# Optimization experiments

Measured on AMD Instinct MI355X. Metric: run time of the kernel, lower is better.

Reference implementation:

```python
import jax, jax.numpy as jnp
import numpy as np

B, N, D_IN, D_OUT, E = 4, 50000, 128, 128, 800000


def setup_inputs() -> dict:
    key = jax.random.key(0)
    k_x, k_w, k_b, k_r, k_c, k_v = jax.random.split(key, 6)
    stdv = 1.0 / np.sqrt(D_OUT)
    x = jax.random.normal(k_x, (B, N, D_IN), dtype=jnp.float32)
    weight = jax.random.uniform(k_w, (D_IN, D_OUT), jnp.float32, -stdv, stdv)
    bias = jax.random.uniform(k_b, (D_OUT,), jnp.float32, -stdv, stdv)
    adj_rows = jax.random.randint(k_r, (E,), 0, N, dtype=jnp.int32)
    adj_cols = jax.random.randint(k_c, (E,), 0, N, dtype=jnp.int32)
    # positive edge weights (e.g. normalized adjacency values)
    adj_vals = jax.random.uniform(k_v, (E,), jnp.float32) * (1.0 / 16.0)
    edge_index = jnp.stack([adj_rows, adj_cols]).astype(jnp.int64)  # unused (pyg_builtin=False)
    return {"input": x, "weight": weight, "bias": bias,
            "adj_vals": adj_vals, "adj_rows": adj_rows, "adj_cols": adj_cols,
            "edge_index": edge_index}


def reference(input, weight, bias, adj_vals, adj_rows, adj_cols, edge_index):
    # support = input @ W : [B, N, D_OUT]
    support = jnp.einsum('bnd,df->bnf', input, weight)

    # node_repr = sparse adj (COO) @ support, batched == torch.sparse.mm path
    def agg(s):  # s: [N, D_OUT]
        msgs = adj_vals[:, None] * s[adj_cols]          # [E, D_OUT] gather
        return jax.ops.segment_sum(msgs, adj_rows, num_segments=N)  # scatter-add

    node_repr = jax.vmap(agg)(support) + bias           # [B, N, D_OUT]
    # net_norm='none' -> no norm; activation=relu; residual=False; dropout=0
    return jax.nn.relu(node_repr)
```

## Files before the change

### kernel.cpp

```cpp
#include <hip/hip_runtime.h>
#include <hip/hip_bf16.h>

#define BB 4
#define NN 50000
#define DIN 128
#define DOUT 128
#define EE 800000
#define TOTROWS (BB * NN)
#define LDA 136

typedef unsigned short u16;
typedef unsigned int u32;

using shortx8 = __attribute__((ext_vector_type(8))) short;
using ushortx4 = __attribute__((ext_vector_type(4))) unsigned short;
using ushortx8 = __attribute__((ext_vector_type(8))) unsigned short;
using floatx4 = __attribute__((ext_vector_type(4))) float;

__device__ __forceinline__ float b2f(u16 u) {
    u32 x = ((u32)u) << 16;
    float f;
    __builtin_memcpy(&f, &x, 4);
    return f;
}

__device__ __forceinline__ u16 f2b(float f) {
    u32 x;
    __builtin_memcpy(&x, &f, 4);
    u32 r = x + 0x7fffu + ((x >> 16) & 1u);
    return (u16)(r >> 16);
}

__global__ __launch_bounds__(256)
void k_detect(const u16* __restrict__ X, const u16* __restrict__ W,
              const u16* __restrict__ Bs, const u16* __restrict__ V,
              int nx, int nw, int nb, int nv, int* __restrict__ flags) {
    __shared__ int cnt[4];
    const int t = threadIdx.x;
    const int w = t >> 6;
    const int l = t & 63;
    if (t < 4) cnt[t] = 0;
    __syncthreads();
    const u16* p = (w == 0) ? X : (w == 1) ? W : (w == 2) ? Bs : V;
    const int n  = (w == 0) ? nx : (w == 1) ? nw : (w == 2) ? nb : nv;
    int bad = 0;
    for (int k = 0; k < 4; ++k) {
        unsigned idx = 2u * (unsigned)(((unsigned long long)(l * 4 + k) *
                                        (unsigned)(n >> 1)) >> 8);
        u16 s = p[idx];
        unsigned e = (s >> 7) & 0xFF;
        bool ok = ((s & 0x7FFF) == 0) || (e >= 90 && e <= 141);
        bad += ok ? 0 : 1;
    }
    atomicAdd(&cnt[w], bad);
    __syncthreads();
    if (l == 0) flags[w] = (cnt[w] >= 77) ? 1 : 0;
}

__global__ __launch_bounds__(256)
void k_prep(const void* __restrict__ Wv, const int* __restrict__ flags,
            u16* __restrict__ Wt) {
    int t = blockIdx.x * 256 + threadIdx.x;
    if (t < DIN * DOUT) {
        int f = t >> 7, k = t & 127;
        size_t src = (size_t)k * DOUT + f;
        Wt[t] = flags[1] ? f2b(((const float*)Wv)[src]) : ((const u16*)Wv)[src];
    }
}

__global__ __launch_bounds__(256, 3)
void k_gemm(const void* __restrict__ Xv, const u16* __restrict__ Wt,
            const int* __restrict__ flags, u16* __restrict__ sup) {
    __shared__ u16 lA[128 * LDA];

    const int xf32 = flags[0];
    const int tid = threadIdx.x;
    const int wid = tid >> 6;
    const int l   = tid & 63;
    const long rowBase = (long)blockIdx.x * 128;

    if (xf32) {
        const float* Xf = (const float*)Xv;
#pragma unroll
        for (int i = 0; i < 16; ++i) {
            int elem = i * 1024 + tid * 4;
            int row = elem >> 7, col = elem & 127;
            long gRow = rowBase + row;
            ushortx4 w4 = (ushortx4){0, 0, 0, 0};
            if (gRow < TOTROWS) {
                float4 v = *(const float4*)(Xf + gRow * DIN + col);
                w4[0] = f2b(v.x); w4[1] = f2b(v.y);
                w4[2] = f2b(v.z); w4[3] = f2b(v.w);
            }
            *(ushortx4*)&lA[row * LDA + col] = w4;
        }
    } else {
        const u16* X16 = (const u16*)Xv;
#pragma unroll
        for (int i = 0; i < 8; ++i) {
            int elem = i * 2048 + tid * 8;
            int row = elem >> 7, col = elem & 127;
            long gRow = rowBase + row;
            ushortx8 w8 = (ushortx8){0, 0, 0, 0, 0, 0, 0, 0};
            if (gRow < TOTROWS)
                w8 = *(const ushortx8*)(X16 + gRow * DIN + col);
            *(ushortx8*)&lA[row * LDA + col] = w8;
        }
    }

    const int wx = wid & 1;
    const int wy = wid >> 1;
    const int q8 = (l >> 4) * 8;
    const int lm = l & 15;

    shortx8 bf[16];
#pragma unroll
    for (int nt = 0; nt < 4; ++nt) {
        const size_t Frow = (size_t)(wx * 64 + nt * 16 + lm) * DIN;
#pragma unroll
        for (int c = 0; c < 4; ++c)
            bf[nt * 4 + c] = *(const shortx8*)(Wt + Frow + 32 * c + q8);
    }

    floatx4 acc[4][4];
#pragma unroll
    for (int mt = 0; mt < 4; ++mt)
#pragma unroll
        for (int nt = 0; nt < 4; ++nt)
            acc[mt][nt] = (floatx4){0.f, 0.f, 0.f, 0.f};

    __syncthreads();

    for (int c = 0; c < 4; ++c) {
        shortx8 af[4];
#pragma unroll
        for (int mt = 0; mt < 4; ++mt)
            af[mt] = *(const shortx8*)
                &lA[(size_t)(wy * 64 + mt * 16 + lm) * LDA + 32 * c + q8];
#pragma unroll
        for (int mt = 0; mt < 4; ++mt)
#pragma unroll
            for (int nt = 0; nt < 4; ++nt)
                acc[mt][nt] = __builtin_amdgcn_mfma_f32_16x16x32_bf16(
                    af[mt], bf[nt * 4 + c], acc[mt][nt], 0, 0, 0);
    }

    __syncthreads();
#pragma unroll
    for (int mt = 0; mt < 4; ++mt) {
#pragma unroll
        for (int reg = 0; reg < 4; ++reg) {
            int row = wy * 64 + mt * 16 + (l >> 4) * 4 + reg;
#pragma unroll
            for (int nt = 0; nt < 4; ++nt)
                lA[row * LDA + wx * 64 + nt * 16 + lm] = f2b(acc[mt][nt][reg]);
        }
    }
    __syncthreads();

#pragma unroll
    for (int i = 0; i < 8; ++i) {
        int elem = i * 2048 + tid * 8;
        int row = elem >> 7, col = elem & 127;
        long R = rowBase + row;
        if (R < TOTROWS) {
            int b = (int)(R / NN);
            int n = (int)(R % NN);
            ushortx8 v = *(const ushortx8*)&lA[row * LDA + col];
            *(ushortx8*)(sup + ((size_t)n * BB + b) * DOUT + col) = v;
        }
    }
}

__global__ __launch_bounds__(256)
void k_hist(const int* __restrict__ rows, int* __restrict__ deg) {
    int e = blockIdx.x * 256 + threadIdx.x;
    if (e < EE) atomicAdd(&deg[rows[e]], 1);
}

#define CHUNK 1024
#define NCHUNK ((NN + CHUNK - 1) / CHUNK)

__global__ __launch_bounds__(256)
void k_scan_reduce(const int* __restrict__ deg, int* __restrict__ bsum) {
    __shared__ int sh[256];
    int t = threadIdx.x, blk = blockIdx.x;
    int base = blk * CHUNK + t * 4;
    int s = 0;
#pragma unroll
    for (int i = 0; i < 4; ++i) {
        int idx = base + i;
        if (idx < NN) s += deg[idx];
    }
    sh[t] = s;
    __syncthreads();
    for (int d = 128; d > 0; d >>= 1) {
        if (t < d) sh[t] += sh[t + d];
        __syncthreads();
    }
    if (t == 0) bsum[blk] = sh[0];
}

__global__ __launch_bounds__(64)
void k_scan_base(const int* __restrict__ bsum, int* __restrict__ bbase,
                 int* __restrict__ off) {
    int l = threadIdx.x;
    int orig = (l < NCHUNK) ? bsum[l] : 0;
    int v = orig;
    for (int d = 1; d < 64; d <<= 1) {
        int x = __shfl_up(v, d);
        if (l >= d) v += x;
    }
    if (l < NCHUNK) bbase[l] = v - orig;
    if (l == NCHUNK - 1) off[NN] = v;
}

__global__ __launch_bounds__(256)
void k_scan_chunk(const int* __restrict__ deg, const int* __restrict__ bbase,
                  int* __restrict__ off) {
    __shared__ int sh[256];
    int t = threadIdx.x;
    int blk = blockIdx.x;
    int base = blk * CHUNK + t * 4;
    int v[4];
    int tsum = 0;
#pragma unroll
    for (int i = 0; i < 4; ++i) {
        int idx = base + i;
        v[i] = (idx < NN) ? deg[idx] : 0;
        tsum += v[i];
    }
    sh[t] = tsum;
    __syncthreads();
    for (int d = 1; d < 256; d <<= 1) {
        int x = (t >= d) ? sh[t - d] : 0;
        __syncthreads();
        sh[t] += x;
        __syncthreads();
    }
    int run = sh[t] - tsum + bbase[blk];
#pragma unroll
    for (int i = 0; i < 4; ++i) {
        int idx = base + i;
        if (idx < NN) off[idx] = run;
        run += v[i];
    }
}

__global__ __launch_bounds__(256)
void k_scatter(const int* __restrict__ rows, const int* __restrict__ cols,
               const void* __restrict__ valsv, const int* __restrict__ flags,
               const int* __restrict__ off, int* __restrict__ cur,
               int2* __restrict__ epk) {
    int e = blockIdx.x * 256 + threadIdx.x;
    if (e < EE) {
        int vf32 = flags[3];
        float v = vf32 ? ((const float*)valsv)[e] : b2f(((const u16*)valsv)[e]);
        int r = rows[e];
        int p = off[r] + atomicAdd(&cur[r], 1);
        epk[p] = make_int2(cols[e], __float_as_int(v));
    }
}

__global__ __launch_bounds__(256)
void k_agg(const u16* __restrict__ sup, const int* __restrict__ off,
           const int2* __restrict__ epk, const void* __restrict__ biasv,
           const int* __restrict__ flags, float* __restrict__ out) {
    const int wid = threadIdx.x >> 6;
    const int l   = threadIdx.x & 63;
    const int n = blockIdx.x * 4 + wid;
    if (n >= NN) return;

    const int p0 = off[n];
    const int p1 = off[n + 1];

    float acc[8] = {0.f, 0.f, 0.f, 0.f, 0.f, 0.f, 0.f, 0.f};
    const int b  = l >> 4;
    const int f0 = (l & 15) * 8;
    const int lofs = l * 8;

    int p = p0;
    for (; p + 4 <= p1; p += 4) {
        int2 e0 = epk[p],     e1 = epk[p + 1];
        int2 e2 = epk[p + 2], e3 = epk[p + 3];
        ushortx8 s0 = *(const ushortx8*)(sup + (size_t)e0.x * 512 + lofs);
        ushortx8 s1 = *(const ushortx8*)(sup + (size_t)e1.x * 512 + lofs);
        ushortx8 s2 = *(const ushortx8*)(sup + (size_t)e2.x * 512 + lofs);
        ushortx8 s3 = *(const ushortx8*)(sup + (size_t)e3.x * 512 + lofs);
        float v0 = __int_as_float(e0.y), v1 = __int_as_float(e1.y);
        float v2 = __int_as_float(e2.y), v3 = __int_as_float(e3.y);
#pragma unroll
        for (int t = 0; t < 8; ++t) acc[t] += v0 * b2f(s0[t]);
#pragma unroll
        for (int t = 0; t < 8; ++t) acc[t] += v1 * b2f(s1[t]);
#pragma unroll
        for (int t = 0; t < 8; ++t) acc[t] += v2 * b2f(s2[t]);
#pragma unroll
        for (int t = 0; t < 8; ++t) acc[t] += v3 * b2f(s3[t]);
    }
    for (; p < p1; ++p) {
        int2 e = epk[p];
        float v = __int_as_float(e.y);
        ushortx8 s = *(const ushortx8*)(sup + (size_t)e.x * 512 + lofs);
#pragma unroll
        for (int t = 0; t < 8; ++t) acc[t] += v * b2f(s[t]);
    }

    float bb[8];
    if (flags[2]) {
        float4 bv1 = *(const float4*)((const float*)biasv + f0);
        float4 bv2 = *(const float4*)((const float*)biasv + f0 + 4);
        bb[0] = bv1.x; bb[1] = bv1.y; bb[2] = bv1.z; bb[3] = bv1.w;
        bb[4] = bv2.x; bb[5] = bv2.y; bb[6] = bv2.z; bb[7] = bv2.w;
    } else {
        ushortx8 bv = *(const ushortx8*)((const u16*)biasv + f0);
#pragma unroll
        for (int t = 0; t < 8; ++t) bb[t] = b2f(bv[t]);
    }

    float r[8];
#pragma unroll
    for (int t = 0; t < 8; ++t) r[t] = fmaxf(acc[t] + bb[t], 0.f);

    float* op = out + ((size_t)b * NN + n) * DOUT + f0;
    *(float4*)op       = (float4){r[0], r[1], r[2], r[3]};
    *(float4*)(op + 4) = (float4){r[4], r[5], r[6], r[7]};
}

extern "C" void kernel_launch(void* const* d_in, const int* in_sizes, int n_in,
                              void* d_out, int out_size, void* d_ws, size_t ws_size,
                              hipStream_t stream) {
    const void* X    = d_in[0];
    const void* W    = d_in[1];
    const void* bias = d_in[2];
    const void* vals = d_in[3];
    const int* rows  = (const int*)d_in[4];
    const int* cols  = (const int*)d_in[5];
    float* out = (float*)d_out;

    char* base = (char*)d_ws;
    size_t o = 0;
    int* flags = (int*)(base + o); o += 64;
    int* deg = (int*)(base + o); o += (size_t)NN * 4;
    int* cur = (int*)(base + o); o += (size_t)NN * 4;
    o = (o + 255) & ~(size_t)255;
    int* bsum  = (int*)(base + o); o += 64 * 4;
    int* bbase = (int*)(base + o); o += 64 * 4;
    o = (o + 255) & ~(size_t)255;
    u16* Wt = (u16*)(base + o); o += (size_t)DIN * DOUT * 2;
    o = (o + 255) & ~(size_t)255;
    int* off = (int*)(base + o); o += (size_t)(NN + 1) * 4;
    o = (o + 255) & ~(size_t)255;
    int2* epk = (int2*)(base + o); o += (size_t)EE * 8;
    o = (o + 255) & ~(size_t)255;
    u16* sup = (u16*)(base + o); o += (size_t)BB * NN * DOUT * 2;
    (void)ws_size;

    hipMemsetAsync(deg, 0, (size_t)2 * NN * 4, stream);

    k_detect<<<1, 256, 0, stream>>>((const u16*)X, (const u16*)W,
                                    (const u16*)bias, (const u16*)vals,
                                    in_sizes[0], in_sizes[1], in_sizes[2],
                                    in_sizes[3], flags);
    k_prep<<<64, 256, 0, stream>>>(W, flags, Wt);
    k_gemm<<<(TOTROWS + 127) / 128, 256, 0, stream>>>(X, Wt, flags, sup);
    k_hist<<<(EE + 255) / 256, 256, 0, stream>>>(rows, deg);
    k_scan_reduce<<<NCHUNK, 256, 0, stream>>>(deg, bsum);
    k_scan_base<<<1, 64, 0, stream>>>(bsum, bbase, off);
    k_scan_chunk<<<NCHUNK, 256, 0, stream>>>(deg, bbase, off);
    k_scatter<<<(EE + 255) / 256, 256, 0, stream>>>(rows, cols, vals, flags,
                                                    off, cur, epk);
    k_agg<<<(NN + 3) / 4, 256, 0, stream>>>(sup, off, epk, bias, flags, out);
}
```

Before: 422.1 us.

## Merge small kernels and pad CSR rows for wave-batched aggregation

Independent kernels are merged by splitting blocks: detect with hist, scan-reduce with weight prep, and GEMM with edge scatter. This cuts the launch count and lets the scatter overlap the GEMM. CSR rows are padded to multiples of 8 and zero-filled, so the aggregation loads up to 64 edges per wave at once, broadcasts them with readlane and issues 8 gathers per step with no tail loop. The cost is an extra memset of the enlarged edge buffer and wasted gathers on padded zero edges, which all point at row 0.

```diff
diff --git a/kernel.cpp b/kernel.cpp
--- a/kernel.cpp
+++ b/kernel.cpp
@@ -9,6 +9,14 @@
 #define TOTROWS (BB * NN)
 #define LDA 136
 
+#define NGB ((TOTROWS + 127) / 128)
+#define NHB ((EE + 255) / 256)
+#define CHUNK 1024
+#define NCHUNK ((NN + CHUNK - 1) / CHUNK)
+#define NPB 64
+#define PAD8(x) (((x) + 7) & ~7)
+#define EPK_CAP (EE + 8 * NN)
+
 typedef unsigned short u16;
 typedef unsigned int u32;
 
@@ -32,45 +40,133 @@
 }
 
 __global__ __launch_bounds__(256)
-void k_detect(const u16* __restrict__ X, const u16* __restrict__ W,
-              const u16* __restrict__ Bs, const u16* __restrict__ V,
-              int nx, int nw, int nb, int nv, int* __restrict__ flags) {
-    __shared__ int cnt[4];
-    const int t = threadIdx.x;
-    const int w = t >> 6;
-    const int l = t & 63;
-    if (t < 4) cnt[t] = 0;
+void k1_detect_hist(const u16* __restrict__ X, const u16* __restrict__ W,
+                    const u16* __restrict__ Bs, const u16* __restrict__ V,
+                    int nx, int nw, int nb, int nv, int* __restrict__ flags,
+                    const int* __restrict__ rows, int* __restrict__ deg) {
+    if (blockIdx.x == 0) {
+        __shared__ int cnt[4];
+        const int t = threadIdx.x;
+        const int w = t >> 6;
+        const int l = t & 63;
+        if (t < 4) cnt[t] = 0;
+        __syncthreads();
+        const u16* p = (w == 0) ? X : (w == 1) ? W : (w == 2) ? Bs : V;
+        const int n  = (w == 0) ? nx : (w == 1) ? nw : (w == 2) ? nb : nv;
+        int bad = 0;
+        for (int k = 0; k < 4; ++k) {
+            unsigned idx = 2u * (unsigned)(((unsigned long long)(l * 4 + k) *
+                                            (unsigned)(n >> 1)) >> 8);
+            u16 s = p[idx];
+            unsigned e = (s >> 7) & 0xFF;
+            bool ok = ((s & 0x7FFF) == 0) || (e >= 90 && e <= 141);
+            bad += ok ? 0 : 1;
+        }
+        atomicAdd(&cnt[w], bad);
+        __syncthreads();
+        if (l == 0) flags[w] = (cnt[w] >= 77) ? 1 : 0;
+    } else {
+        int e = (int)(blockIdx.x - 1) * 256 + threadIdx.x;
+        if (e < EE) atomicAdd(&deg[rows[e]], 1);
+    }
+}
+
+__global__ __launch_bounds__(256)
+void k2_scanred_prep(const int* __restrict__ deg, int* __restrict__ bsum,
+                     const void* __restrict__ Wv, const int* __restrict__ flags,
+                     u16* __restrict__ Wt) {
+    if (blockIdx.x < NCHUNK) {
+        __shared__ int sh[256];
+        int t = threadIdx.x, blk = blockIdx.x;
+        int base = blk * CHUNK + t * 4;
+        int s = 0;
+#pragma unroll
+        for (int i = 0; i < 4; ++i) {
+            int idx = base + i;
+            if (idx < NN) s += PAD8(deg[idx]);
+        }
+        sh[t] = s;
+        __syncthreads();
+        for (int d = 128; d > 0; d >>= 1) {
+            if (t < d) sh[t] += sh[t + d];
+            __syncthreads();
+        }
+        if (t == 0) bsum[blk] = sh[0];
+    } else {
+        int t = (int)(blockIdx.x - NCHUNK) * 256 + threadIdx.x;
+        if (t < DIN * DOUT) {
+            int f = t >> 7, k = t & 127;
+            size_t src = (size_t)k * DOUT + f;
+            Wt[t] = flags[1] ? f2b(((const float*)Wv)[src]) : ((const u16*)Wv)[src];
+        }
+    }
+}
+
+__global__ __launch_bounds__(64)
+void k_scan_base(const int* __restrict__ bsum, int* __restrict__ bbase,
+                 int* __restrict__ off) {
+    int l = threadIdx.x;
+    int orig = (l < NCHUNK) ? bsum[l] : 0;
+    int v = orig;
+    for (int d = 1; d < 64; d <<= 1) {
+        int x = __shfl_up(v, d);
+        if (l >= d) v += x;
+    }
+    if (l < NCHUNK) bbase[l] = v - orig;
+    if (l == NCHUNK - 1) off[NN] = v;
+}
+
+__global__ __launch_bounds__(256)
+void k_scan_chunk(const int* __restrict__ deg, const int* __restrict__ bbase,
+                  int* __restrict__ off) {
+    __shared__ int sh[256];
+    int t = threadIdx.x;
+    int blk = blockIdx.x;
+    int base = blk * CHUNK + t * 4;
+    int v[4];
+    int tsum = 0;
+#pragma unroll
+    for (int i = 0; i < 4; ++i) {
+        int idx = base + i;
+        v[i] = (idx < NN) ? PAD8(deg[idx]) : 0;
+        tsum += v[i];
+    }
+    sh[t] = tsum;
     __syncthreads();
-    const u16* p = (w == 0) ? X : (w == 1) ? W : (w == 2) ? Bs : V;
-    const int n  = (w == 0) ? nx : (w == 1) ? nw : (w == 2) ? nb : nv;
-    int bad = 0;
-    for (int k = 0; k < 4; ++k) {
-        unsigned idx = 2u * (unsigned)(((unsigned long long)(l * 4 + k) *
-                                        (unsigned)(n >> 1)) >> 8);
-        u16 s = p[idx];
-        unsigned e = (s >> 7) & 0xFF;
-        bool ok = ((s & 0x7FFF) == 0) || (e >= 90 && e <= 141);
-        bad += ok ? 0 : 1;
-    }
-    atomicAdd(&cnt[w], bad);
-    __syncthreads();
-    if (l == 0) flags[w] = (cnt[w] >= 77) ? 1 : 0;
-}
-
-__global__ __launch_bounds__(256)
-void k_prep(const void* __restrict__ Wv, const int* __restrict__ flags,
-            u16* __restrict__ Wt) {
-    int t = blockIdx.x * 256 + threadIdx.x;
-    if (t < DIN * DOUT) {
-        int f = t >> 7, k = t & 127;
-        size_t src = (size_t)k * DOUT + f;
-        Wt[t] = flags[1] ? f2b(((const float*)Wv)[src]) : ((const u16*)Wv)[src];
+    for (int d = 1; d < 256; d <<= 1) {
+        int x = (t >= d) ? sh[t - d] : 0;
+        __syncthreads();
+        sh[t] += x;
+        __syncthreads();
+    }
+    int run = sh[t] - tsum + bbase[blk];
+#pragma unroll
+    for (int i = 0; i < 4; ++i) {
+        int idx = base + i;
+        if (idx < NN) off[idx] = run;
+        run += v[i];
     }
 }
 
 __global__ __launch_bounds__(256, 3)
-void k_gemm(const void* __restrict__ Xv, const u16* __restrict__ Wt,
-            const int* __restrict__ flags, u16* __restrict__ sup) {
+void k5_gemm_scatter(const void* __restrict__ Xv, const u16* __restrict__ Wt,
+                     const int* __restrict__ flags, u16* __restrict__ sup,
+                     const int* __restrict__ rows, const int* __restrict__ cols,
+                     const void* __restrict__ valsv, const int* __restrict__ off,
+                     int* __restrict__ cur, int2* __restrict__ epk) {
+    if (blockIdx.x >= NGB) {
+        int e = (int)(blockIdx.x - NGB) * 256 + threadIdx.x;
+        if (e < EE) {
+            int vf32 = flags[3];
+            float v = vf32 ? ((const float*)valsv)[e]
+                           : b2f(((const u16*)valsv)[e]);
+            int r = rows[e];
+            int p = off[r] + atomicAdd(&cur[r], 1);
+            epk[p] = make_int2(cols[e], __float_as_int(v));
+        }
+        return;
+    }
+
     __shared__ u16 lA[128 * LDA];
 
     const int xf32 = flags[0];
@@ -173,96 +269,6 @@
 }
 
 __global__ __launch_bounds__(256)
-void k_hist(const int* __restrict__ rows, int* __restrict__ deg) {
-    int e = blockIdx.x * 256 + threadIdx.x;
-    if (e < EE) atomicAdd(&deg[rows[e]], 1);
-}
-
-#define CHUNK 1024
-#define NCHUNK ((NN + CHUNK - 1) / CHUNK)
-
-__global__ __launch_bounds__(256)
-void k_scan_reduce(const int* __restrict__ deg, int* __restrict__ bsum) {
-    __shared__ int sh[256];
-    int t = threadIdx.x, blk = blockIdx.x;
-    int base = blk * CHUNK + t * 4;
-    int s = 0;
-#pragma unroll
-    for (int i = 0; i < 4; ++i) {
-        int idx = base + i;
-        if (idx < NN) s += deg[idx];
-    }
-    sh[t] = s;
-    __syncthreads();
-    for (int d = 128; d > 0; d >>= 1) {
-        if (t < d) sh[t] += sh[t + d];
-        __syncthreads();
-    }
-    if (t == 0) bsum[blk] = sh[0];
-}
-
-__global__ __launch_bounds__(64)
-void k_scan_base(const int* __restrict__ bsum, int* __restrict__ bbase,
-                 int* __restrict__ off) {
-    int l = threadIdx.x;
-    int orig = (l < NCHUNK) ? bsum[l] : 0;
-    int v = orig;
-    for (int d = 1; d < 64; d <<= 1) {
-        int x = __shfl_up(v, d);
-        if (l >= d) v += x;
-    }
-    if (l < NCHUNK) bbase[l] = v - orig;
-    if (l == NCHUNK - 1) off[NN] = v;
-}
-
-__global__ __launch_bounds__(256)
-void k_scan_chunk(const int* __restrict__ deg, const int* __restrict__ bbase,
-                  int* __restrict__ off) {
-    __shared__ int sh[256];
-    int t = threadIdx.x;
-    int blk = blockIdx.x;
-    int base = blk * CHUNK + t * 4;
-    int v[4];
-    int tsum = 0;
-#pragma unroll
-    for (int i = 0; i < 4; ++i) {
-        int idx = base + i;
-        v[i] = (idx < NN) ? deg[idx] : 0;
-        tsum += v[i];
-    }
-    sh[t] = tsum;
-    __syncthreads();
-    for (int d = 1; d < 256; d <<= 1) {
-        int x = (t >= d) ? sh[t - d] : 0;
-        __syncthreads();
-        sh[t] += x;
-        __syncthreads();
-    }
-    int run = sh[t] - tsum + bbase[blk];
-#pragma unroll
-    for (int i = 0; i < 4; ++i) {
-        int idx = base + i;
-        if (idx < NN) off[idx] = run;
-        run += v[i];
-    }
-}
-
-__global__ __launch_bounds__(256)
-void k_scatter(const int* __restrict__ rows, const int* __restrict__ cols,
-               const void* __restrict__ valsv, const int* __restrict__ flags,
-               const int* __restrict__ off, int* __restrict__ cur,
-               int2* __restrict__ epk) {
-    int e = blockIdx.x * 256 + threadIdx.x;
-    if (e < EE) {
-        int vf32 = flags[3];
-        float v = vf32 ? ((const float*)valsv)[e] : b2f(((const u16*)valsv)[e]);
-        int r = rows[e];
-        int p = off[r] + atomicAdd(&cur[r], 1);
-        epk[p] = make_int2(cols[e], __float_as_int(v));
-    }
-}
-
-__global__ __launch_bounds__(256)
 void k_agg(const u16* __restrict__ sup, const int* __restrict__ off,
            const int2* __restrict__ epk, const void* __restrict__ biasv,
            const int* __restrict__ flags, float* __restrict__ out) {
@@ -271,39 +277,36 @@
     const int n = blockIdx.x * 4 + wid;
     if (n >= NN) return;
 
-    const int p0 = off[n];
-    const int p1 = off[n + 1];
+    const int p0 = __builtin_amdgcn_readfirstlane(off[n]);
+    const int p1 = __builtin_amdgcn_readfirstlane(off[n + 1]);
 
     float acc[8] = {0.f, 0.f, 0.f, 0.f, 0.f, 0.f, 0.f, 0.f};
     const int b  = l >> 4;
     const int f0 = (l & 15) * 8;
     const int lofs = l * 8;
 
-    int p = p0;
-    for (; p + 4 <= p1; p += 4) {
-        int2 e0 = epk[p],     e1 = epk[p + 1];
-        int2 e2 = epk[p + 2], e3 = epk[p + 3];
-        ushortx8 s0 = *(const ushortx8*)(sup + (size_t)e0.x * 512 + lofs);
-        ushortx8 s1 = *(const ushortx8*)(sup + (size_t)e1.x * 512 + lofs);
-        ushortx8 s2 = *(const ushortx8*)(sup + (size_t)e2.x * 512 + lofs);
-        ushortx8 s3 = *(const ushortx8*)(sup + (size_t)e3.x * 512 + lofs);
-        float v0 = __int_as_float(e0.y), v1 = __int_as_float(e1.y);
-        float v2 = __int_as_float(e2.y), v3 = __int_as_float(e3.y);
-#pragma unroll
-        for (int t = 0; t < 8; ++t) acc[t] += v0 * b2f(s0[t]);
-#pragma unroll
-        for (int t = 0; t < 8; ++t) acc[t] += v1 * b2f(s1[t]);
-#pragma unroll
-        for (int t = 0; t < 8; ++t) acc[t] += v2 * b2f(s2[t]);
-#pragma unroll
-        for (int t = 0; t < 8; ++t) acc[t] += v3 * b2f(s3[t]);
-    }
-    for (; p < p1; ++p) {
-        int2 e = epk[p];
-        float v = __int_as_float(e.y);
-        ushortx8 s = *(const ushortx8*)(sup + (size_t)e.x * 512 + lofs);
-#pragma unroll
-        for (int t = 0; t < 8; ++t) acc[t] += v * b2f(s[t]);
+    for (int pb = p0; pb < p1; pb += 64) {
+        const int cnt = min(64, p1 - pb);
+        int2 d = make_int2(0, 0);
+        if (l < cnt) d = epk[pb + l];
+        for (int j = 0; j < cnt; j += 8) {
+            int   cs[8];
+            float vs[8];
+#pragma unroll
+            for (int q = 0; q < 8; ++q) {
+                cs[q] = __builtin_amdgcn_readlane(d.x, j + q);
+                vs[q] = __int_as_float(__builtin_amdgcn_readlane(d.y, j + q));
+            }
+            ushortx8 sv[8];
+#pragma unroll
+            for (int q = 0; q < 8; ++q)
+                sv[q] = *(const ushortx8*)(sup + (size_t)cs[q] * 512 + lofs);
+#pragma unroll
+            for (int q = 0; q < 8; ++q)
+#pragma unroll
+                for (int t = 0; t < 8; ++t)
+                    acc[t] += vs[q] * b2f(sv[q][t]);
+        }
     }
 
     float bb[8];
@@ -351,24 +354,21 @@
     o = (o + 255) & ~(size_t)255;
     int* off = (int*)(base + o); o += (size_t)(NN + 1) * 4;
     o = (o + 255) & ~(size_t)255;
-    int2* epk = (int2*)(base + o); o += (size_t)EE * 8;
+    int2* epk = (int2*)(base + o); o += (size_t)EPK_CAP * 8;
     o = (o + 255) & ~(size_t)255;
     u16* sup = (u16*)(base + o); o += (size_t)BB * NN * DOUT * 2;
     (void)ws_size;
 
     hipMemsetAsync(deg, 0, (size_t)2 * NN * 4, stream);
-
-    k_detect<<<1, 256, 0, stream>>>((const u16*)X, (const u16*)W,
-                                    (const u16*)bias, (const u16*)vals,
-                                    in_sizes[0], in_sizes[1], in_sizes[2],
-                                    in_sizes[3], flags);
-    k_prep<<<64, 256, 0, stream>>>(W, flags, Wt);
-    k_gemm<<<(TOTROWS + 127) / 128, 256, 0, stream>>>(X, Wt, flags, sup);
-    k_hist<<<(EE + 255) / 256, 256, 0, stream>>>(rows, deg);
-    k_scan_reduce<<<NCHUNK, 256, 0, stream>>>(deg, bsum);
+    hipMemsetAsync(epk, 0, (size_t)EPK_CAP * 8, stream);
+
+    k1_detect_hist<<<1 + NHB, 256, 0, stream>>>(
+        (const u16*)X, (const u16*)W, (const u16*)bias, (const u16*)vals,
+        in_sizes[0], in_sizes[1], in_sizes[2], in_sizes[3], flags, rows, deg);
+    k2_scanred_prep<<<NCHUNK + NPB, 256, 0, stream>>>(deg, bsum, W, flags, Wt);
     k_scan_base<<<1, 64, 0, stream>>>(bsum, bbase, off);
     k_scan_chunk<<<NCHUNK, 256, 0, stream>>>(deg, bbase, off);
-    k_scatter<<<(EE + 255) / 256, 256, 0, stream>>>(rows, cols, vals, flags,
-                                                    off, cur, epk);
+    k5_gemm_scatter<<<NGB + NHB, 256, 0, stream>>>(
+        X, Wt, flags, sup, rows, cols, vals, off, cur, epk);
     k_agg<<<(NN + 3) / 4, 256, 0, stream>>>(sup, off, epk, bias, flags, out);
 }
```

Result: faster. 405.9 us (-3.8%).
